# Kernel optimization log

Measured on AMD Instinct MI355X. Metric: run time of the kernel, lower is better.

## Reference

```python
import jax, jax.numpy as jnp
import numpy as np

# ultralytics ops.non_max_suppression defaults
CONF_THRES = 0.25
IOU_THRES = 0.45
MAX_DET = 300          # max detections returned per image
MAX_WH = 7680.0        # class-offset constant for class-aware NMS
MAX_NMS = 1024         # fixed candidate cap (ultralytics uses 30000; fixed-size for jit)


def _xywh2xyxy(x):
    # x: [..., 4] (cx, cy, w, h) -> (x1, y1, x2, y2)
    xy, half_wh = x[..., :2], x[..., 2:] * 0.5
    return jnp.concatenate([xy - half_wh, xy + half_wh], axis=-1)


def _pairwise_iou(b):
    # b: [K, 4] xyxy -> [K, K] IoU
    area = (b[:, 2] - b[:, 0]) * (b[:, 3] - b[:, 1])
    lt = jnp.maximum(b[:, None, :2], b[None, :, :2])
    rb = jnp.minimum(b[:, None, 2:], b[None, :, 2:])
    wh = jnp.clip(rb - lt, 0.0)
    inter = wh[..., 0] * wh[..., 1]
    return inter / (area[:, None] + area[None, :] - inter + 1e-7)


def _nms_single(pred):
    # pred: [4+nc, N] raw detector output for one image
    boxes = _xywh2xyxy(pred[:4].T)          # [N, 4]
    scores = pred[4:].T                     # [N, nc]
    conf = scores.max(axis=-1)              # [N]
    cls = scores.argmax(axis=-1).astype(pred.dtype)  # [N]

    valid = conf > CONF_THRES
    masked_conf = jnp.where(valid, conf, -1.0)
    top_conf, idx = jax.lax.top_k(masked_conf, MAX_NMS)   # sorted desc
    b = boxes[idx]                          # [K, 4]
    c = cls[idx]                            # [K]

    # class-aware NMS via coordinate offset per class
    iou = _pairwise_iou(b + c[:, None] * MAX_WH)          # [K, K]

    keep0 = top_conf > CONF_THRES
    ar = jnp.arange(MAX_NMS)

    def body(i, keep):
        # greedy: if box i is kept, suppress all lower-scored boxes with high IoU
        sup = keep[i] & (iou[i] > IOU_THRES) & (ar > i)
        return keep & ~sup

    keep = jax.lax.fori_loop(0, MAX_NMS, body, keep0)

    kept_conf = jnp.where(keep, top_conf, -1.0)
    det_conf, di = jax.lax.top_k(kept_conf, MAX_DET)
    det = jnp.concatenate(
        [b[di], det_conf[:, None], c[di][:, None]], axis=-1)  # [MAX_DET, 6]
    ok = (det_conf > CONF_THRES)[:, None]
    return jnp.where(ok, det, 0.0)


def setup_inputs() -> dict:
    key = jax.random.key(0)
    # [batch, 4+nc, num_anchors]: xywh in [0,1), class scores in [0,1)
    preds = jax.random.uniform(key, (32, 84, 8400), dtype=jnp.float32)
    return {"preds": preds}


def reference(preds):
    dets = jax.vmap(_nms_single)(preds)  # [B, MAX_DET, 6] (xyxy, conf, cls)
    return dets[0]                       # module returns preds[0]
```

## Files before the change

### kernel.cpp

```cpp
#include <hip/hip_runtime.h>
#include <cstdint>
#include <cstddef>


#define NA    8400
#define NCLS  80
#define NTOP  1024
#define NDET  300
#define CONF_T 0.25f
#define IOU_T  0.45f
#define MAXWH  7680.0f

#define NSLICE 25
#define SLICEW 336

#define OFF_KEY   0
#define OFF_CLS   33600
#define OFF_CONF  67200
#define OFF_SCONF 100800
#define OFF_SX1   104896
#define OFF_SY1   108992
#define OFF_SX2   113088
#define OFF_SY2   117184
#define OFF_SCLS  121280
#define OFF_SUP   125376
#define OFF_RANK  256448

__device__ __forceinline__ int sw(int j) { return j + (j >> 6); }

__global__ __launch_bounds__(256) void k_confcls(const float* __restrict__ pred,
                                                 unsigned int* __restrict__ key,
                                                 float* __restrict__ clsf,
                                                 float* __restrict__ conf,
                                                 unsigned int* __restrict__ rank)
{
    int a = blockIdx.x * 256 + threadIdx.x;
    if (a >= NA) return;
    const float* s = pred + 4 * NA;
    float best = s[a];
    int bc = 0;
#pragma unroll 16
    for (int c = 1; c < NCLS; ++c) {
        float v = s[c * NA + a];
        if (v > best) { best = v; bc = c; }
    }
    float m = (best > CONF_T) ? best : -1.0f;
    unsigned int u = __float_as_uint(m);
    unsigned int mono = u ^ ((u & 0x80000000u) ? 0xFFFFFFFFu : 0x80000000u);
    key[a]  = ~mono;
    clsf[a] = (float)bc;
    conf[a] = m;
    rank[a] = 0u;
}

__global__ __launch_bounds__(256) void k_rank_partial(const unsigned int* __restrict__ key,
                                                      unsigned int* __restrict__ rank)
{
    __shared__ __align__(16) unsigned int kh[SLICEW];
    int tid = threadIdx.x;
    int s   = blockIdx.y;
    int jb  = s * SLICEW;
    if (tid < SLICEW - 256 + 256) {}
    for (int k = tid; k < SLICEW; k += 256) kh[k] = key[jb + k];
    __syncthreads();

    int a = blockIdx.x * 256 + tid;
    if (a >= NA) return;

    unsigned long long myk = (((unsigned long long)key[a]) << 32) | (unsigned int)a;
    unsigned int r = 0;
    const uint4* kv4 = (const uint4*)kh;
#pragma unroll 4
    for (int j4 = 0; j4 < SLICEW / 4; ++j4) {
        uint4 kk = kv4[j4];
        unsigned int j = (unsigned int)jb + (unsigned int)j4 * 4u;
        r += ((((unsigned long long)kk.x) << 32) | (j + 0u)) < myk;
        r += ((((unsigned long long)kk.y) << 32) | (j + 1u)) < myk;
        r += ((((unsigned long long)kk.z) << 32) | (j + 2u)) < myk;
        r += ((((unsigned long long)kk.w) << 32) | (j + 3u)) < myk;
    }
    atomicAdd(&rank[a], r);
}

__global__ __launch_bounds__(256) void k_scatter(const float* __restrict__ pred,
                                                 const unsigned int* __restrict__ rank,
                                                 const float* __restrict__ clsf,
                                                 const float* __restrict__ conf,
                                                 float* __restrict__ wsf)
{
    int a = blockIdx.x * 256 + threadIdx.x;
    if (a >= NA) return;
    unsigned int r = rank[a];
    if (r < NTOP) {
#pragma clang fp contract(off)
        float x = pred[0 * NA + a], y = pred[1 * NA + a];
        float w = pred[2 * NA + a], h = pred[3 * NA + a];
        float hw = w * 0.5f, hh = h * 0.5f;
        wsf[OFF_SCONF / 4 + r] = conf[a];
        wsf[OFF_SX1  / 4 + r] = x - hw;
        wsf[OFF_SY1  / 4 + r] = y - hh;
        wsf[OFF_SX2  / 4 + r] = x + hw;
        wsf[OFF_SY2  / 4 + r] = y + hh;
        wsf[OFF_SCLS / 4 + r] = clsf[a];
    }
}

__global__ __launch_bounds__(256) void k_supmat(const float* __restrict__ wsf,
                                                unsigned long long* __restrict__ sup)
{
#pragma clang fp contract(off)
    __shared__ float ox1[NTOP + 16], oy1[NTOP + 16];
    __shared__ float ox2[NTOP + 16], oy2[NTOP + 16];
    __shared__ float oar[NTOP + 16];
    int tid = threadIdx.x;
    for (int k = tid; k < NTOP; k += 256) {
        float cls = wsf[OFF_SCLS / 4 + k];
        float off = cls * MAXWH;
        float x1 = wsf[OFF_SX1 / 4 + k] + off;
        float y1 = wsf[OFF_SY1 / 4 + k] + off;
        float x2 = wsf[OFF_SX2 / 4 + k] + off;
        float y2 = wsf[OFF_SY2 / 4 + k] + off;
        int si = sw(k);
        ox1[si] = x1; oy1[si] = y1; ox2[si] = x2; oy2[si] = y2;
        oar[si] = (x2 - x1) * (y2 - y1);
    }
    __syncthreads();

    int gid = blockIdx.x * 256 + tid;
    int i = gid >> 4;
    int l = gid & 15;
    int si = sw(i);
    float bx1 = ox1[si], by1 = oy1[si], bx2 = ox2[si], by2 = oy2[si], ba = oar[si];
    unsigned long long bits = 0ULL;
    int j0 = l << 6;
#pragma unroll 4
    for (int jj = 0; jj < 64; ++jj) {
        int j = j0 + jj;
        int sj = sw(j);
        float xx1 = fmaxf(bx1, ox1[sj]);
        float yy1 = fmaxf(by1, oy1[sj]);
        float xx2 = fminf(bx2, ox2[sj]);
        float yy2 = fminf(by2, oy2[sj]);
        float w  = fmaxf(xx2 - xx1, 0.0f);
        float hh = fmaxf(yy2 - yy1, 0.0f);
        float inter = w * hh;
        float denom = ba + oar[sj] - inter + 1e-7f;
        bool s = (j > i) && ((inter / denom) > IOU_T);
        bits |= ((unsigned long long)s) << jj;
    }
    sup[(size_t)i * 16 + l] = bits;
}

__global__ __launch_bounds__(512) void k_nms_out(const float* __restrict__ wsf,
                                                 const unsigned long long* __restrict__ sup,
                                                 float* __restrict__ out)
{
    __shared__ unsigned long long kc[16];
    __shared__ unsigned int pcs[16];
    int tid  = threadIdx.x;
    int lane = tid & 63;
    int wv   = tid >> 6;

    const float* sconf = wsf + OFF_SCONF / 4;
    unsigned long long b1 = __ballot(sconf[tid] > CONF_T);
    unsigned long long b2 = __ballot(sconf[512 + tid] > CONF_T);
    if (lane == 0) { kc[wv] = b1; kc[8 + wv] = b2; }
    __syncthreads();

    if (wv == 0) {
        unsigned long long keep = (lane < 16) ? kc[lane] : 0ULL;
        int l = lane & 15;
        for (int g = 0; g < 16; ++g) {
            unsigned long long cur = __shfl(keep, g);
            const unsigned long long* base = sup + (size_t)g * 64 * 16;
#pragma unroll 16
            for (int ii = 0; ii < 64; ++ii) {
                unsigned long long rl = base[ii * 16 + l];
                unsigned long long rg = base[ii * 16 + g];
                unsigned long long sel = 0ULL - ((cur >> ii) & 1ULL);
                keep &= ~(rl & sel);
                cur  &= ~(rg & sel);
            }
        }
        if (lane < 16) kc[lane] = keep;
    }
    __syncthreads();

    if (tid < 16) pcs[tid] = (unsigned int)__popcll(kc[tid]);
    __syncthreads();

    if (tid < NDET) {
        int acc = 0, chunk = -1, off = 0;
#pragma unroll
        for (int c = 0; c < 16; ++c) {
            int p = (int)pcs[c];
            if (chunk < 0 && tid < acc + p) { chunk = c; off = tid - acc; }
            acc += p;
        }
        float o0 = 0.f, o1 = 0.f, o2 = 0.f, o3 = 0.f, o4 = 0.f, o5 = 0.f;
        if (chunk >= 0) {
            unsigned long long m = kc[chunk];
            for (int q = 0; q < off; ++q) m &= m - 1ULL;
            int p = chunk * 64 + __builtin_ctzll(m);
            o0 = wsf[OFF_SX1  / 4 + p];
            o1 = wsf[OFF_SY1  / 4 + p];
            o2 = wsf[OFF_SX2  / 4 + p];
            o3 = wsf[OFF_SY2  / 4 + p];
            o4 = wsf[OFF_SCONF / 4 + p];
            o5 = wsf[OFF_SCLS / 4 + p];
        }
        out[tid * 6 + 0] = o0; out[tid * 6 + 1] = o1; out[tid * 6 + 2] = o2;
        out[tid * 6 + 3] = o3; out[tid * 6 + 4] = o4; out[tid * 6 + 5] = o5;
    }
}

extern "C" void kernel_launch(void* const* d_in, const int* in_sizes, int n_in,
                              void* d_out, int out_size, void* d_ws, size_t ws_size,
                              hipStream_t stream)
{
    const float* preds = (const float*)d_in[0];
    char* ws = (char*)d_ws;
    unsigned int* key  = (unsigned int*)(ws + OFF_KEY);
    float* clsf        = (float*)(ws + OFF_CLS);
    float* conf        = (float*)(ws + OFF_CONF);
    float* wsf         = (float*)ws;
    unsigned long long* sup  = (unsigned long long*)(ws + OFF_SUP);
    unsigned int* rank = (unsigned int*)(ws + OFF_RANK);
    float* out = (float*)d_out;

    hipLaunchKernelGGL(k_confcls,      dim3(33),         dim3(256), 0, stream, preds, key, clsf, conf, rank);
    hipLaunchKernelGGL(k_rank_partial, dim3(33, NSLICE), dim3(256), 0, stream, key, rank);
    hipLaunchKernelGGL(k_scatter,      dim3(33),         dim3(256), 0, stream, preds, rank, clsf, conf, wsf);
    hipLaunchKernelGGL(k_supmat,       dim3(64),         dim3(256), 0, stream, wsf, sup);
    hipLaunchKernelGGL(k_nms_out,      dim3(1),          dim3(512), 0, stream, wsf, sup, out);
}
```

Measured before the change: 206.7 us.

## Split class argmax across four waves and software-pipeline greedy NMS scan

The confidence/class kernel now uses 1024 threads per block, with four groups each scanning 20 classes. The partial maxima are packed into 64-bit keys and reduced in shared memory, giving the class stage four times as many threads. The serial greedy NMS loop now runs on 16 lanes and double-buffers suppression-matrix rows in registers (A/B blocks of 16 rows), prefetching the next block while processing the current one. Cross-lane row broadcasts use readlane instead of a second global load, aiming to hide load latency in the single-block sequential scan at the cost of more registers.

```diff
diff --git a/kernel.cpp b/kernel.cpp
--- a/kernel.cpp
+++ b/kernel.cpp
@@ -26,71 +26,101 @@
 #define OFF_SUP   125376
 #define OFF_RANK  256448
 
+typedef unsigned long long u64;
+typedef unsigned int u32;
+
 __device__ __forceinline__ int sw(int j) { return j + (j >> 6); }
 
-__global__ __launch_bounds__(256) void k_confcls(const float* __restrict__ pred,
-                                                 unsigned int* __restrict__ key,
-                                                 float* __restrict__ clsf,
-                                                 float* __restrict__ conf,
-                                                 unsigned int* __restrict__ rank)
-{
-    int a = blockIdx.x * 256 + threadIdx.x;
-    if (a >= NA) return;
-    const float* s = pred + 4 * NA;
-    float best = s[a];
-    int bc = 0;
-#pragma unroll 16
-    for (int c = 1; c < NCLS; ++c) {
-        float v = s[c * NA + a];
-        if (v > best) { best = v; bc = c; }
-    }
-    float m = (best > CONF_T) ? best : -1.0f;
-    unsigned int u = __float_as_uint(m);
-    unsigned int mono = u ^ ((u & 0x80000000u) ? 0xFFFFFFFFu : 0x80000000u);
-    key[a]  = ~mono;
-    clsf[a] = (float)bc;
-    conf[a] = m;
-    rank[a] = 0u;
-}
-
-__global__ __launch_bounds__(256) void k_rank_partial(const unsigned int* __restrict__ key,
-                                                      unsigned int* __restrict__ rank)
-{
-    __shared__ __align__(16) unsigned int kh[SLICEW];
+__device__ __forceinline__ u32 f2mono(float f) {
+    u32 u = __float_as_uint(f);
+    return u ^ ((u & 0x80000000u) ? 0xFFFFFFFFu : 0x80000000u);
+}
+__device__ __forceinline__ float mono2f(u32 m) {
+    u32 u = (m & 0x80000000u) ? (m ^ 0x80000000u) : ~m;
+    return __uint_as_float(u);
+}
+__device__ __forceinline__ u64 rl64(u64 v, int g) {
+    u32 lo = (u32)__builtin_amdgcn_readlane((int)(u32)v, g);
+    u32 hi = (u32)__builtin_amdgcn_readlane((int)(u32)(v >> 32), g);
+    return ((u64)hi << 32) | lo;
+}
+
+__global__ __launch_bounds__(1024) void k_confcls(const float* __restrict__ pred,
+                                                  u32* __restrict__ key,
+                                                  float* __restrict__ clsf,
+                                                  float* __restrict__ conf,
+                                                  u32* __restrict__ rank)
+{
+    __shared__ u64 pk[4][256];
+    int tid = threadIdx.x;
+    int q = tid >> 8, t = tid & 255;
+    int a = blockIdx.x * 256 + t;
+    u64 pv = 0ULL;
+    if (a < NA) {
+        const float* s = pred + 4 * NA + (size_t)(q * 20) * NA;
+        float best = s[a];
+        int bc = q * 20;
+#pragma unroll
+        for (int c = 1; c < 20; ++c) {
+            float v = s[(size_t)c * NA + a];
+            if (v > best) { best = v; bc = q * 20 + c; }
+        }
+        pv = ((u64)f2mono(best) << 32) | (u32)(255 - bc);
+    }
+    pk[q][t] = pv;
+    __syncthreads();
+    if (q == 0 && a < NA) {
+        u64 m0 = pk[0][t], m1 = pk[1][t], m2 = pk[2][t], m3 = pk[3][t];
+        u64 mm = m0 > m1 ? m0 : m1;
+        u64 nn = m2 > m3 ? m2 : m3;
+        if (nn > mm) mm = nn;
+        float best = mono2f((u32)(mm >> 32));
+        int bc = 255 - (int)(mm & 0xFFu);
+        float m = (best > CONF_T) ? best : -1.0f;
+        key[a]  = ~f2mono(m);
+        clsf[a] = (float)bc;
+        conf[a] = m;
+        rank[a] = 0u;
+    }
+}
+
+__global__ __launch_bounds__(256) void k_rank_partial(const u32* __restrict__ key,
+                                                      u32* __restrict__ rank)
+{
+    __shared__ __align__(16) u32 kh[SLICEW];
     int tid = threadIdx.x;
     int s   = blockIdx.y;
     int jb  = s * SLICEW;
-    if (tid < SLICEW - 256 + 256) {}
     for (int k = tid; k < SLICEW; k += 256) kh[k] = key[jb + k];
     __syncthreads();
 
     int a = blockIdx.x * 256 + tid;
     if (a >= NA) return;
 
-    unsigned long long myk = (((unsigned long long)key[a]) << 32) | (unsigned int)a;
-    unsigned int r = 0;
+    u64 myk = (((u64)key[a]) << 32) | (u32)a;
+    u32 r = 0;
     const uint4* kv4 = (const uint4*)kh;
 #pragma unroll 4
     for (int j4 = 0; j4 < SLICEW / 4; ++j4) {
         uint4 kk = kv4[j4];
-        unsigned int j = (unsigned int)jb + (unsigned int)j4 * 4u;
-        r += ((((unsigned long long)kk.x) << 32) | (j + 0u)) < myk;
-        r += ((((unsigned long long)kk.y) << 32) | (j + 1u)) < myk;
-        r += ((((unsigned long long)kk.z) << 32) | (j + 2u)) < myk;
-        r += ((((unsigned long long)kk.w) << 32) | (j + 3u)) < myk;
+        u32 j = (u32)jb + (u32)j4 * 4u;
+        r += ((((u64)kk.x) << 32) | (j + 0u)) < myk;
+        r += ((((u64)kk.y) << 32) | (j + 1u)) < myk;
+        r += ((((u64)kk.z) << 32) | (j + 2u)) < myk;
+        r += ((((u64)kk.w) << 32) | (j + 3u)) < myk;
     }
     atomicAdd(&rank[a], r);
 }
 
 __global__ __launch_bounds__(256) void k_scatter(const float* __restrict__ pred,
-                                                 const unsigned int* __restrict__ rank,
+                                                 const u32* __restrict__ rank,
                                                  const float* __restrict__ clsf,
                                                  const float* __restrict__ conf,
                                                  float* __restrict__ wsf)
 {
     int a = blockIdx.x * 256 + threadIdx.x;
     if (a >= NA) return;
-    unsigned int r = rank[a];
+    u32 r = rank[a];
     if (r < NTOP) {
 #pragma clang fp contract(off)
         float x = pred[0 * NA + a], y = pred[1 * NA + a];
@@ -106,7 +136,7 @@
 }
 
 __global__ __launch_bounds__(256) void k_supmat(const float* __restrict__ wsf,
-                                                unsigned long long* __restrict__ sup)
+                                                u64* __restrict__ sup)
 {
 #pragma clang fp contract(off)
     __shared__ float ox1[NTOP + 16], oy1[NTOP + 16];
@@ -131,7 +161,7 @@
     int l = gid & 15;
     int si = sw(i);
     float bx1 = ox1[si], by1 = oy1[si], bx2 = ox2[si], by2 = oy2[si], ba = oar[si];
-    unsigned long long bits = 0ULL;
+    u64 bits = 0ULL;
     int j0 = l << 6;
 #pragma unroll 4
     for (int jj = 0; jj < 64; ++jj) {
@@ -146,47 +176,77 @@
         float inter = w * hh;
         float denom = ba + oar[sj] - inter + 1e-7f;
         bool s = (j > i) && ((inter / denom) > IOU_T);
-        bits |= ((unsigned long long)s) << jj;
+        bits |= ((u64)s) << jj;
     }
     sup[(size_t)i * 16 + l] = bits;
 }
 
 __global__ __launch_bounds__(512) void k_nms_out(const float* __restrict__ wsf,
-                                                 const unsigned long long* __restrict__ sup,
+                                                 const u64* __restrict__ sup,
                                                  float* __restrict__ out)
 {
-    __shared__ unsigned long long kc[16];
-    __shared__ unsigned int pcs[16];
+    __shared__ u64 kc[16];
+    __shared__ u32 pcs[16];
     int tid  = threadIdx.x;
     int lane = tid & 63;
     int wv   = tid >> 6;
 
     const float* sconf = wsf + OFF_SCONF / 4;
-    unsigned long long b1 = __ballot(sconf[tid] > CONF_T);
-    unsigned long long b2 = __ballot(sconf[512 + tid] > CONF_T);
+    u64 b1 = __ballot(sconf[tid] > CONF_T);
+    u64 b2 = __ballot(sconf[512 + tid] > CONF_T);
     if (lane == 0) { kc[wv] = b1; kc[8 + wv] = b2; }
     __syncthreads();
 
-    if (wv == 0) {
-        unsigned long long keep = (lane < 16) ? kc[lane] : 0ULL;
-        int l = lane & 15;
-        for (int g = 0; g < 16; ++g) {
-            unsigned long long cur = __shfl(keep, g);
-            const unsigned long long* base = sup + (size_t)g * 64 * 16;
-#pragma unroll 16
-            for (int ii = 0; ii < 64; ++ii) {
-                unsigned long long rl = base[ii * 16 + l];
-                unsigned long long rg = base[ii * 16 + g];
-                unsigned long long sel = 0ULL - ((cur >> ii) & 1ULL);
-                keep &= ~(rl & sel);
-                cur  &= ~(rg & sel);
+    if (wv == 0 && lane < 16) {
+        int l = lane;
+        u64 keep = kc[l];
+        u64 cur = 0ULL;
+        u64 A[16], B[16];
+#pragma unroll
+        for (int k = 0; k < 16; ++k) A[k] = sup[(size_t)k * 16 + l];
+
+        for (int m2 = 0; m2 < 32; ++m2) {
+            int m = m2 * 2;
+#pragma unroll
+            for (int k = 0; k < 16; ++k) B[k] = sup[(size_t)((m + 1) * 16 + k) * 16 + l];
+            {
+                int g = m >> 2;
+                if ((m & 3) == 0) cur = rl64(keep, g);
+                u64 rg[16];
+#pragma unroll
+                for (int k = 0; k < 16; ++k) rg[k] = rl64(A[k], g);
+#pragma unroll
+                for (int k = 0; k < 16; ++k) {
+                    int ii = ((m & 3) << 4) + k;
+                    u64 sel = 0ULL - ((cur >> ii) & 1ULL);
+                    keep &= ~(A[k] & sel);
+                    cur  &= ~(rg[k] & sel);
+                }
             }
-        }
-        if (lane < 16) kc[lane] = keep;
-    }
-    __syncthreads();
-
-    if (tid < 16) pcs[tid] = (unsigned int)__popcll(kc[tid]);
+            if (m2 < 31) {
+#pragma unroll
+                for (int k = 0; k < 16; ++k) A[k] = sup[(size_t)((m + 2) * 16 + k) * 16 + l];
+            }
+            {
+                int mb = m + 1;
+                int g = mb >> 2;
+                u64 rg[16];
+#pragma unroll
+                for (int k = 0; k < 16; ++k) rg[k] = rl64(B[k], g);
+#pragma unroll
+                for (int k = 0; k < 16; ++k) {
+                    int ii = ((mb & 3) << 4) + k;
+                    u64 sel = 0ULL - ((cur >> ii) & 1ULL);
+                    keep &= ~(B[k] & sel);
+                    cur  &= ~(rg[k] & sel);
+                }
+            }
+        }
+        kc[l] = keep;
+    }
+    __syncthreads();
+
+    if (tid < 16) pcs[tid] = (u32)__popcll(kc[tid]);
     __syncthreads();
 
     if (tid < NDET) {
@@ -199,9 +259,9 @@
         }
         float o0 = 0.f, o1 = 0.f, o2 = 0.f, o3 = 0.f, o4 = 0.f, o5 = 0.f;
         if (chunk >= 0) {
-            unsigned long long m = kc[chunk];
-            for (int q = 0; q < off; ++q) m &= m - 1ULL;
-            int p = chunk * 64 + __builtin_ctzll(m);
+            u64 mk = kc[chunk];
+            for (int q = 0; q < off; ++q) mk &= mk - 1ULL;
+            int p = chunk * 64 + __builtin_ctzll(mk);
             o0 = wsf[OFF_SX1  / 4 + p];
             o1 = wsf[OFF_SY1  / 4 + p];
             o2 = wsf[OFF_SX2  / 4 + p];
@@ -220,17 +280,17 @@
 {
     const float* preds = (const float*)d_in[0];
     char* ws = (char*)d_ws;
-    unsigned int* key  = (unsigned int*)(ws + OFF_KEY);
-    float* clsf        = (float*)(ws + OFF_CLS);
-    float* conf        = (float*)(ws + OFF_CONF);
-    float* wsf         = (float*)ws;
-    unsigned long long* sup  = (unsigned long long*)(ws + OFF_SUP);
-    unsigned int* rank = (unsigned int*)(ws + OFF_RANK);
-    float* out = (float*)d_out;
-
-    hipLaunchKernelGGL(k_confcls,      dim3(33),         dim3(256), 0, stream, preds, key, clsf, conf, rank);
-    hipLaunchKernelGGL(k_rank_partial, dim3(33, NSLICE), dim3(256), 0, stream, key, rank);
-    hipLaunchKernelGGL(k_scatter,      dim3(33),         dim3(256), 0, stream, preds, rank, clsf, conf, wsf);
-    hipLaunchKernelGGL(k_supmat,       dim3(64),         dim3(256), 0, stream, wsf, sup);
-    hipLaunchKernelGGL(k_nms_out,      dim3(1),          dim3(512), 0, stream, wsf, sup, out);
-}
+    u32* key    = (u32*)(ws + OFF_KEY);
+    float* clsf = (float*)(ws + OFF_CLS);
+    float* conf = (float*)(ws + OFF_CONF);
+    float* wsf  = (float*)ws;
+    u64* sup    = (u64*)(ws + OFF_SUP);
+    u32* rank   = (u32*)(ws + OFF_RANK);
+    float* out  = (float*)d_out;
+
+    hipLaunchKernelGGL(k_confcls,      dim3(33),         dim3(1024), 0, stream, preds, key, clsf, conf, rank);
+    hipLaunchKernelGGL(k_rank_partial, dim3(33, NSLICE), dim3(256),  0, stream, key, rank);
+    hipLaunchKernelGGL(k_scatter,      dim3(33),         dim3(256),  0, stream, preds, rank, clsf, conf, wsf);
+    hipLaunchKernelGGL(k_supmat,       dim3(64),         dim3(256),  0, stream, wsf, sup);
+    hipLaunchKernelGGL(k_nms_out,      dim3(1),          dim3(512),  0, stream, wsf, sup, out);
+}
```

After: 173.3 us. 1.19x faster.
